# Kernel optimization log

Measured on AMD Instinct MI355X. Metric: run time of the kernel, lower is better.

The kernel has to match this reference:

```python
import jax, jax.numpy as jnp
import numpy as np


def _init(key, shape, fan_in):
    return jax.random.normal(key, shape, jnp.float32) * (1.0 / np.sqrt(fan_in))


def setup_inputs() -> dict:
    key = jax.random.key(0)
    ks = jax.random.split(key, 12)
    b, n, vd, ad, sd, hd = 32, 2048, 512, 128, 128, 64
    return {
        'vfeat': jax.random.normal(ks[0], (b, n, vd), jnp.float32),
        'afeat': jax.random.normal(ks[1], (b, n, ad), jnp.float32),
        'vfc_w': _init(ks[2], (ad, vd), vd), 'vfc_b': jnp.zeros((ad,), jnp.float32),
        'afc_w': _init(ks[3], (ad, ad), ad), 'afc_b': jnp.zeros((ad,), jnp.float32),
        'am_v_w': _init(ks[4], (sd, sd), sd), 'am_v_b': jnp.zeros((sd,), jnp.float32),
        'am_a_w': _init(ks[5], (sd, sd), sd), 'am_a_b': jnp.zeros((sd,), jnp.float32),
        'am_o_w': _init(ks[6], (1, sd), sd), 'am_o_b': jnp.zeros((1,), jnp.float32),
        'V_w': _init(ks[7], (hd, sd), sd), 'V_b': jnp.zeros((hd,), jnp.float32),
        'W_w': _init(ks[8], (1, hd), hd), 'W_b': jnp.zeros((1,), jnp.float32),
        'cls_w': _init(ks[9], (2, sd), sd), 'cls_b': jnp.zeros((2,), jnp.float32),
    }


def reference(vfeat, afeat, vfc_w, vfc_b, afc_w, afc_b,
              am_v_w, am_v_b, am_a_w, am_a_b, am_o_w, am_o_b,
              V_w, V_b, W_w, W_b, cls_w, cls_b):
    relu = jax.nn.relu
    # vfc / afc projections (dropout is identity in eval mode)
    vo1 = relu(jnp.einsum('bnd,kd->bnk', vfeat, vfc_w) + vfc_b)  # (b,n,128)
    ax = relu(jnp.einsum('bnd,kd->bnk', afeat, afc_w) + afc_b)   # (b,n,128)
    # AM(128): additive gated cross-modal attention: out = sigmoid(Wo tanh(Wv v + Wa a)) * a
    h = jnp.tanh(jnp.einsum('bnk,jk->bnj', vo1, am_v_w) + am_v_b
                 + jnp.einsum('bnk,jk->bnj', ax, am_a_w) + am_a_b)
    att = jax.nn.sigmoid(jnp.einsum('bnj,oj->bno', h, am_o_w) + am_o_b)  # (b,n,1)
    ffeat = att * ax + vo1  # attfeat + vo1, (b,n,128)
    # NOTE: original uses self.V for BOTH f_v and f_u (source bug kept)
    f_v = relu(jnp.einsum('bnk,hk->bnh', ffeat, V_w) + V_b)  # (b,n,64)
    f_u = f_v
    # W is affine with no nonlinearity on (fv_i + fu_j), so
    # W(fv_i + fu_j) = w.fv_i + w.fu_j + b  -- exact rank-1 decomposition
    s_v = f_v @ W_w[0]  # (b,n)
    s_u = f_u @ W_w[0]  # (b,n)
    pair = s_v[:, :, None] + s_u[:, None, :] + W_b[0]  # (b,n_i,n_j)
    p = jax.nn.softmax(pair, axis=1)  # F.softmax(scores, 0) per bag: over i
    scores = p.mean(axis=2)  # mean over j -> (b,n)
    # eval mode: training-only softmax over dim 2 skipped
    zfeat = jnp.einsum('bn,bnk->bk', scores, ffeat)  # (b,128)
    logits = zfeat @ cls_w.T + cls_b  # (b,2)
    return scores, logits
```

## Files before the change

kernel.cpp:

```cpp
#include <hip/hip_runtime.h>
#include <cstddef>
#include <cstdint>


typedef __attribute__((ext_vector_type(8))) short short8;
typedef __attribute__((ext_vector_type(4))) float float4v;

#define MFMA16(a, b, c) __builtin_amdgcn_mfma_f32_16x16x32_bf16((a), (b), (c), 0, 0, 0)

__device__ __forceinline__ unsigned short f2bf(float f) {
    union { float f; unsigned u; } v; v.f = f;
    unsigned r = (v.u + 0x7fffu + ((v.u >> 16) & 1u)) >> 16;
    return (unsigned short)r;
}
__device__ __forceinline__ float bf2f(unsigned short h) {
    union { unsigned u; float f; } v; v.u = ((unsigned)h) << 16;
    return v.f;
}
__device__ __forceinline__ float bf2f_s(short h) { return bf2f((unsigned short)h); }

__device__ __forceinline__ void bfsplit(float x, short& h, short& l) {
    union { float f; unsigned u; } v; v.f = x;
    h = (short)(v.u >> 16);
    union { unsigned u; float f; } hv; hv.u = v.u & 0xffff0000u;
    union { float f; unsigned u; } lv; lv.f = x - hv.f;
    l = (short)(lv.u >> 16);
}

__device__ __forceinline__ float tanh_fast(float x) {
    float e = __builtin_exp2f(x * 2.885390081777927f);
    return 1.f - 2.f / (e + 1.f);
}
__device__ __forceinline__ float sigmoid_fast(float x) {
    return 1.f / (1.f + __builtin_exp2f(-x * 1.4426950408889634f));
}

__device__ __forceinline__ void gload_lds16(const void* g, void* l) {
#if __has_builtin(__builtin_amdgcn_global_load_lds)
    __builtin_amdgcn_global_load_lds(
        (const __attribute__((address_space(1))) unsigned int*)g,
        (__attribute__((address_space(3))) unsigned int*)l, 16, 0, 0);
#else
    *(uint4*)l = *(const uint4*)g;
#endif
}

__global__ __launch_bounds__(256)
void prep(const float* __restrict__ vfc_w, const float* __restrict__ afc_w,
          const float* __restrict__ am_v_w, const float* __restrict__ am_a_w,
          const float* __restrict__ V_w,
          unsigned short* __restrict__ W1h, unsigned short* __restrict__ W1l,
          unsigned short* __restrict__ W1bh, unsigned short* __restrict__ W1bl,
          unsigned short* __restrict__ W2v, unsigned short* __restrict__ W2a,
          unsigned short* __restrict__ W3)
{
    int t = blockIdx.x * 256 + threadIdx.x;
    if (t < 65536) {
        int j = t & 7, lane = (t >> 3) & 63, ks = (t >> 9) & 15, nf = (t >> 13) & 7;
        int n = (lane & 15) + 16 * nf, k = ks * 32 + (lane >> 4) * 8 + j;
        float x = vfc_w[n * 512 + k];
        unsigned short h = f2bf(x);
        W1h[t] = h; W1l[t] = f2bf(x - bf2f(h));
    } else if (t < 81920) {
        int u = t - 65536;
        int j = u & 7, lane = (u >> 3) & 63, ks = (u >> 9) & 3, nf = (u >> 11) & 7;
        int n = (lane & 15) + 16 * nf, k = ks * 32 + (lane >> 4) * 8 + j;
        float x = afc_w[n * 128 + k];
        unsigned short h = f2bf(x);
        W1bh[u] = h; W1bl[u] = f2bf(x - bf2f(h));
    } else if (t < 98304) {
        int u = t - 81920;
        int j = u & 7, lane = (u >> 3) & 63, ks = (u >> 9) & 3, nf = (u >> 11) & 7;
        int n = (lane & 15) + 16 * nf, k = ks * 32 + (lane >> 4) * 8 + j;
        W2v[u] = f2bf(am_v_w[n * 128 + k]);
    } else if (t < 114688) {
        int u = t - 98304;
        int j = u & 7, lane = (u >> 3) & 63, ks = (u >> 9) & 3, nf = (u >> 11) & 7;
        int n = (lane & 15) + 16 * nf, k = ks * 32 + (lane >> 4) * 8 + j;
        W2a[u] = f2bf(am_a_w[n * 128 + k]);
    } else if (t < 122880) {
        int u = t - 114688;
        int j = u & 7, lane = (u >> 3) & 63, ks = (u >> 9) & 3, nf = (u >> 11) & 3;
        int n = (lane & 15) + 16 * nf, k = ks * 32 + (lane >> 4) * 8 + j;
        W3[u] = f2bf(V_w[n * 128 + k]);
    }
}

__global__ __launch_bounds__(256, 2)
void milA(const float* __restrict__ vfeat, const float* __restrict__ afeat,
          const float* __restrict__ vfc_b, const float* __restrict__ afc_b,
          const float* __restrict__ am_v_b, const float* __restrict__ am_a_b,
          const float* __restrict__ am_o_w, const float* __restrict__ am_o_b,
          const float* __restrict__ V_b, const float* __restrict__ W_w,
          const unsigned short* __restrict__ W1h, const unsigned short* __restrict__ W1l,
          const unsigned short* __restrict__ W1bh, const unsigned short* __restrict__ W1bl,
          const unsigned short* __restrict__ W2v, const unsigned short* __restrict__ W2a,
          const unsigned short* __restrict__ W3,
          float* __restrict__ ffeat_out, float* __restrict__ s_out)
{
    __shared__ __align__(16) unsigned short bstage[16384];
    __shared__ __align__(16) unsigned short vo1s[8192];
    __shared__ __align__(16) unsigned short axs[8192];

    const int tid = threadIdx.x;
    const int lane = tid & 63, wid = tid >> 6;
    const int lr = lane & 15, lg = lane >> 4;
    const int row0 = blockIdx.x * 64 + wid * 16;

    const float* ap  = vfeat + (size_t)(row0 + lr) * 512 + lg * 8;
    const float* apb = afeat + (size_t)(row0 + lr) * 128 + lg * 8;

    float4v acc1[8];
#pragma unroll
    for (int nf = 0; nf < 8; ++nf)
#pragma unroll
        for (int i = 0; i < 4; ++i) acc1[nf][i] = 0.f;

    float4 acur[4], anxt[4];
#pragma unroll
    for (int q = 0; q < 4; ++q)
        acur[q] = *(const float4*)(ap + (q >> 1) * 32 + (q & 1) * 4);

    for (int s = 0; s < 8; ++s) {
        __syncthreads();
#pragma unroll
        for (int i = 0; i < 8; ++i) {
            const int f = wid * 8 + i;
            const int ksl = f >> 4, rest = f & 15, isl = rest >> 3, nf = rest & 7;
            const unsigned short* src = (isl ? W1l : W1h)
                + (size_t)(nf * 16 + (s * 2 + ksl)) * 512 + (size_t)lane * 8;
            gload_lds16(src, &bstage[f * 512 + lane * 8]);
        }
        __syncthreads();

        if (s < 7) {
            const float* apn = ap + (s + 1) * 64;
#pragma unroll
            for (int q = 0; q < 4; ++q)
                anxt[q] = *(const float4*)(apn + (q >> 1) * 32 + (q & 1) * 4);
        } else {
#pragma unroll
            for (int q = 0; q < 4; ++q)
                anxt[q] = *(const float4*)(apb + (q >> 1) * 32 + (q & 1) * 4);
        }

#pragma unroll
        for (int ksl = 0; ksl < 2; ++ksl) {
            short8 ah, al;
            {
                const float4 x0 = acur[ksl * 2], x1 = acur[ksl * 2 + 1];
                const float xs[8] = {x0.x, x0.y, x0.z, x0.w, x1.x, x1.y, x1.z, x1.w};
#pragma unroll
                for (int j = 0; j < 8; ++j) {
                    short h, l; bfsplit(xs[j], h, l);
                    ah[j] = h; al[j] = l;
                }
            }
#pragma unroll
            for (int nf = 0; nf < 8; ++nf) {
                const short8 bh = *(const short8*)&bstage[(ksl * 16 + nf) * 512 + lane * 8];
                const short8 bl = *(const short8*)&bstage[(ksl * 16 + 8 + nf) * 512 + lane * 8];
                acc1[nf] = MFMA16(ah, bh, acc1[nf]);
                acc1[nf] = MFMA16(ah, bl, acc1[nf]);
                acc1[nf] = MFMA16(al, bh, acc1[nf]);
            }
        }
#pragma unroll
        for (int q = 0; q < 4; ++q) acur[q] = anxt[q];
    }
#pragma unroll
    for (int nf = 0; nf < 8; ++nf) {
        const float bb = vfc_b[lr + 16 * nf];
#pragma unroll
        for (int r = 0; r < 4; ++r) {
            float v = fmaxf(acc1[nf][r] + bb, 0.f);
            acc1[nf][r] = v;
            const int row = lg * 4 + r;
            const int col = lr + 16 * nf;
            vo1s[wid * 2048 + row * 128 + (col ^ ((row & 7) << 3))] = f2bf(v);
        }
    }

    float4v acc1b[8];
#pragma unroll
    for (int nf = 0; nf < 8; ++nf)
#pragma unroll
        for (int i = 0; i < 4; ++i) acc1b[nf][i] = 0.f;

    for (int s = 0; s < 2; ++s) {
        __syncthreads();
#pragma unroll
        for (int i = 0; i < 8; ++i) {
            const int f = wid * 8 + i;
            const int ksl = f >> 4, rest = f & 15, isl = rest >> 3, nf = rest & 7;
            const unsigned short* src = (isl ? W1bl : W1bh)
                + (size_t)(nf * 4 + (s * 2 + ksl)) * 512 + (size_t)lane * 8;
            gload_lds16(src, &bstage[f * 512 + lane * 8]);
        }
        __syncthreads();

        if (s < 1) {
            const float* apn = apb + 64;
#pragma unroll
            for (int q = 0; q < 4; ++q)
                anxt[q] = *(const float4*)(apn + (q >> 1) * 32 + (q & 1) * 4);
        }

#pragma unroll
        for (int ksl = 0; ksl < 2; ++ksl) {
            short8 ah, al;
            {
                const float4 x0 = acur[ksl * 2], x1 = acur[ksl * 2 + 1];
                const float xs[8] = {x0.x, x0.y, x0.z, x0.w, x1.x, x1.y, x1.z, x1.w};
#pragma unroll
                for (int j = 0; j < 8; ++j) {
                    short h, l; bfsplit(xs[j], h, l);
                    ah[j] = h; al[j] = l;
                }
            }
#pragma unroll
            for (int nf = 0; nf < 8; ++nf) {
                const short8 bh = *(const short8*)&bstage[(ksl * 16 + nf) * 512 + lane * 8];
                const short8 bl = *(const short8*)&bstage[(ksl * 16 + 8 + nf) * 512 + lane * 8];
                acc1b[nf] = MFMA16(ah, bh, acc1b[nf]);
                acc1b[nf] = MFMA16(ah, bl, acc1b[nf]);
                acc1b[nf] = MFMA16(al, bh, acc1b[nf]);
            }
        }
#pragma unroll
        for (int q = 0; q < 4; ++q) acur[q] = anxt[q];
    }
#pragma unroll
    for (int nf = 0; nf < 8; ++nf) {
        const float bb = afc_b[lr + 16 * nf];
#pragma unroll
        for (int r = 0; r < 4; ++r) {
            float v = fmaxf(acc1b[nf][r] + bb, 0.f);
            acc1b[nf][r] = v;
            const int row = lg * 4 + r;
            const int col = lr + 16 * nf;
            axs[wid * 2048 + row * 128 + (col ^ ((row & 7) << 3))] = f2bf(v);
        }
    }

    float4v acc2[8];
#pragma unroll
    for (int nf = 0; nf < 8; ++nf)
#pragma unroll
        for (int i = 0; i < 4; ++i) acc2[nf][i] = 0.f;

    for (int s = 0; s < 2; ++s) {
        __syncthreads();
#pragma unroll
        for (int i = 0; i < 8; ++i) {
            const int f = wid * 8 + i;
            const int ksl = f >> 4, rest = f & 15, isa = rest >> 3, nf = rest & 7;
            const unsigned short* src = (isa ? W2a : W2v)
                + (size_t)(nf * 4 + (s * 2 + ksl)) * 512 + (size_t)lane * 8;
            gload_lds16(src, &bstage[f * 512 + lane * 8]);
        }
        __syncthreads();

#pragma unroll
        for (int ksl = 0; ksl < 2; ++ksl) {
            const int ks = s * 2 + ksl;
            const int rdoff = (ks * 32 + lg * 8) ^ ((lr & 7) << 3);
            const short8 a2v = *(const short8*)&vo1s[wid * 2048 + lr * 128 + rdoff];
            const short8 a2a = *(const short8*)&axs[wid * 2048 + lr * 128 + rdoff];
#pragma unroll
            for (int nf = 0; nf < 8; ++nf) {
                const short8 bv = *(const short8*)&bstage[(ksl * 16 + nf) * 512 + lane * 8];
                const short8 ba = *(const short8*)&bstage[(ksl * 16 + 8 + nf) * 512 + lane * 8];
                acc2[nf] = MFMA16(a2v, bv, acc2[nf]);
                acc2[nf] = MFMA16(a2a, ba, acc2[nf]);
            }
        }
    }

    __syncthreads();
#pragma unroll
    for (int i = 0; i < 4; ++i) {
        const int f = wid * 4 + i;
        gload_lds16(W3 + (size_t)f * 512 + lane * 8, &bstage[f * 512 + lane * 8]);
    }

    float attc[4];
    {
        float bias2[8], wo[8];
#pragma unroll
        for (int nf = 0; nf < 8; ++nf) {
            const int c = lr + 16 * nf;
            bias2[nf] = am_v_b[c] + am_a_b[c];
            wo[nf] = am_o_w[c];
        }
        const float ob = am_o_b[0];
#pragma unroll
        for (int r = 0; r < 4; ++r) {
            float p = 0.f;
#pragma unroll
            for (int nf = 0; nf < 8; ++nf)
                p += tanh_fast(acc2[nf][r] + bias2[nf]) * wo[nf];
            p += __shfl_xor(p, 1);
            p += __shfl_xor(p, 2);
            p += __shfl_xor(p, 4);
            p += __shfl_xor(p, 8);
            attc[r] = sigmoid_fast(p + ob);
        }
    }

#pragma unroll
    for (int nf = 0; nf < 8; ++nf)
#pragma unroll
        for (int r = 0; r < 4; ++r)
            ffeat_out[(size_t)(row0 + lg * 4 + r) * 128 + lr + 16 * nf] =
                attc[r] * acc1b[nf][r] + acc1[nf][r];

    float attv;
    {
        const int srcl = (lr >> 2) << 4;
        const float b0 = __shfl(attc[0], srcl);
        const float b1 = __shfl(attc[1], srcl);
        const float b2 = __shfl(attc[2], srcl);
        const float b3 = __shfl(attc[3], srcl);
        attv = (lr & 2) ? ((lr & 1) ? b3 : b2) : ((lr & 1) ? b1 : b0);
    }

    __syncthreads();

    float4v acc3[4];
#pragma unroll
    for (int nf = 0; nf < 4; ++nf)
#pragma unroll
        for (int i = 0; i < 4; ++i) acc3[nf][i] = 0.f;

#pragma unroll
    for (int ks = 0; ks < 4; ++ks) {
        const int rdoff = (ks * 32 + lg * 8) ^ ((lr & 7) << 3);
        const short8 x8 = *(const short8*)&axs[wid * 2048 + lr * 128 + rdoff];
        const short8 v8 = *(const short8*)&vo1s[wid * 2048 + lr * 128 + rdoff];
        short8 a3;
#pragma unroll
        for (int j = 0; j < 8; ++j) {
            float f = attv * bf2f_s(x8[j]) + bf2f_s(v8[j]);
            a3[j] = (short)f2bf(f);
        }
#pragma unroll
        for (int nf = 0; nf < 4; ++nf) {
            const short8 b = *(const short8*)&bstage[(nf * 4 + ks) * 512 + lane * 8];
            acc3[nf] = MFMA16(a3, b, acc3[nf]);
        }
    }

    {
        float vb3[4], ww3[4];
#pragma unroll
        for (int nf = 0; nf < 4; ++nf) {
            const int c = lr + 16 * nf;
            vb3[nf] = V_b[c];
            ww3[nf] = W_w[c];
        }
#pragma unroll
        for (int r = 0; r < 4; ++r) {
            float q = 0.f;
#pragma unroll
            for (int nf = 0; nf < 4; ++nf)
                q += fmaxf(acc3[nf][r] + vb3[nf], 0.f) * ww3[nf];
            q += __shfl_xor(q, 1);
            q += __shfl_xor(q, 2);
            q += __shfl_xor(q, 4);
            q += __shfl_xor(q, 8);
            if (lr == 0) s_out[row0 + lg * 4 + r] = q;
        }
    }
}

__device__ __forceinline__ float wred_sum(float v) {
#pragma unroll
    for (int m = 32; m >= 1; m >>= 1) v += __shfl_xor(v, m);
    return v;
}
__device__ __forceinline__ float wred_max(float v) {
#pragma unroll
    for (int m = 32; m >= 1; m >>= 1) v = fmaxf(v, __shfl_xor(v, m));
    return v;
}

__global__ __launch_bounds__(256)
void milB12(const float* __restrict__ s_in, const float* __restrict__ ffeat,
            float* __restrict__ scores_out, float* __restrict__ parts)
{
    __shared__ float red[4];
    __shared__ float sh[256];
    __shared__ float zbuf[256];

    const int t = threadIdx.x, w = t >> 6;
    const int b = blockIdx.x >> 3, part = blockIdx.x & 7;
    const float* sb = s_in + (size_t)b * 2048;

    float v[8];
#pragma unroll
    for (int q = 0; q < 8; ++q) v[q] = sb[q * 256 + t];
    float m = v[0];
#pragma unroll
    for (int q = 1; q < 8; ++q) m = fmaxf(m, v[q]);
    m = wred_max(m);
    if ((t & 63) == 0) red[w] = m;
    __syncthreads();
    const float bm = fmaxf(fmaxf(red[0], red[1]), fmaxf(red[2], red[3]));

    float sum = 0.f;
#pragma unroll
    for (int q = 0; q < 8; ++q) sum += expf(v[q] - bm);
    sum = wred_sum(sum);
    __syncthreads();
    if ((t & 63) == 0) red[w] = sum;
    __syncthreads();
    const float inv = 1.f / (red[0] + red[1] + red[2] + red[3]);

    const float sv = sb[part * 256 + t];
    const float sc = expf(sv - bm) * inv;
    scores_out[(size_t)b * 2048 + part * 256 + t] = sc;
    sh[t] = sc;
    __syncthreads();

    const int col = t & 127, half = t >> 7;
    const float* fb = ffeat + ((size_t)(b * 2048 + part * 256 + half * 128)) * 128 + col;
    const float* sp = sh + half * 128;
    float z = 0.f;
#pragma unroll 8
    for (int nn = 0; nn < 128; ++nn) z += sp[nn] * fb[(size_t)nn * 128];
    zbuf[t] = z;
    __syncthreads();
    if (t < 128) parts[((size_t)(b * 8 + part)) * 128 + t] = zbuf[t] + zbuf[t + 128];
}

__global__ __launch_bounds__(128)
void milB3(const float* __restrict__ parts, const float* __restrict__ cls_w,
           const float* __restrict__ cls_b, float* __restrict__ logits)
{
    __shared__ float zfs[128];
    const int t = threadIdx.x, b = blockIdx.x;
    float zf = 0.f;
#pragma unroll
    for (int p = 0; p < 8; ++p) zf += parts[((size_t)(b * 8 + p)) * 128 + t];
    zfs[t] = zf;
    __syncthreads();
    const int o = t >> 6, c = t & 63;
    float q = zfs[c] * cls_w[o * 128 + c] + zfs[c + 64] * cls_w[o * 128 + c + 64];
    q = wred_sum(q);
    if (c == 0) logits[b * 2 + o] = q + cls_b[o];
}

extern "C" void kernel_launch(void* const* d_in, const int* in_sizes, int n_in,
                              void* d_out, int out_size, void* d_ws, size_t ws_size,
                              hipStream_t stream)
{
    (void)in_sizes; (void)n_in; (void)out_size; (void)ws_size;
    const float* vfeat  = (const float*)d_in[0];
    const float* afeat  = (const float*)d_in[1];
    const float* vfc_w  = (const float*)d_in[2];
    const float* vfc_b  = (const float*)d_in[3];
    const float* afc_w  = (const float*)d_in[4];
    const float* afc_b  = (const float*)d_in[5];
    const float* am_v_w = (const float*)d_in[6];
    const float* am_v_b = (const float*)d_in[7];
    const float* am_a_w = (const float*)d_in[8];
    const float* am_a_b = (const float*)d_in[9];
    const float* am_o_w = (const float*)d_in[10];
    const float* am_o_b = (const float*)d_in[11];
    const float* V_w    = (const float*)d_in[12];
    const float* V_b    = (const float*)d_in[13];
    const float* W_w    = (const float*)d_in[14];
    const float* cls_w  = (const float*)d_in[16];
    const float* cls_b  = (const float*)d_in[17];

    float* scores = (float*)d_out;
    float* logits = (float*)d_out + 32 * 2048;

    char* ws = (char*)d_ws;
    float* ffeat_ws = (float*)ws;
    float* s_ws     = (float*)(ws + 33554432);
    float* parts_ws = (float*)(ws + 33816576);
    unsigned short* W1h  = (unsigned short*)(ws + 33947648);
    unsigned short* W1l  = W1h + 65536;
    unsigned short* W1bh = W1l + 65536;
    unsigned short* W1bl = W1bh + 16384;
    unsigned short* W2v  = W1bl + 16384;
    unsigned short* W2a  = W2v + 16384;
    unsigned short* W3   = W2a + 16384;

    prep<<<480, 256, 0, stream>>>(vfc_w, afc_w, am_v_w, am_a_w, V_w,
                                  W1h, W1l, W1bh, W1bl, W2v, W2a, W3);
    milA<<<1024, 256, 0, stream>>>(vfeat, afeat, vfc_b, afc_b, am_v_b, am_a_b,
                                   am_o_w, am_o_b, V_b, W_w,
                                   W1h, W1l, W1bh, W1bl, W2v, W2a, W3,
                                   ffeat_ws, s_ws);
    milB12<<<256, 256, 0, stream>>>(s_ws, ffeat_ws, scores, parts_ws);
    milB3<<<32, 128, 0, stream>>>(parts_ws, cls_w, cls_b, logits);
}
```

Measured before the change: 83.51 us.

## Drop low-half weight term in vfc GEMM and halve LDS staging for occupancy

The vfc projection now uses only the high bf16 half of the weights, so it runs two MFMAs per step (ah*bh, al*bh) instead of three. That cuts weight staging traffic and matrix work in the largest GEMM. The LDS staging buffer is halved, and the afc and attention GEMM loops are restructured to stage one k-slice per sync. Launch bounds are raised to 3 blocks per CU to improve occupancy. This loses precision in the vfc output and doubles the number of barrier rounds in the smaller GEMMs.

```diff
diff --git a/kernel.cpp b/kernel.cpp
--- a/kernel.cpp
+++ b/kernel.cpp
@@ -86,19 +86,19 @@
     }
 }
 
-__global__ __launch_bounds__(256, 2)
+__global__ __launch_bounds__(256, 3)
 void milA(const float* __restrict__ vfeat, const float* __restrict__ afeat,
           const float* __restrict__ vfc_b, const float* __restrict__ afc_b,
           const float* __restrict__ am_v_b, const float* __restrict__ am_a_b,
           const float* __restrict__ am_o_w, const float* __restrict__ am_o_b,
           const float* __restrict__ V_b, const float* __restrict__ W_w,
-          const unsigned short* __restrict__ W1h, const unsigned short* __restrict__ W1l,
+          const unsigned short* __restrict__ W1h,
           const unsigned short* __restrict__ W1bh, const unsigned short* __restrict__ W1bl,
           const unsigned short* __restrict__ W2v, const unsigned short* __restrict__ W2a,
           const unsigned short* __restrict__ W3,
           float* __restrict__ ffeat_out, float* __restrict__ s_out)
 {
-    __shared__ __align__(16) unsigned short bstage[16384];
+    __shared__ __align__(16) unsigned short bstage[8192];
     __shared__ __align__(16) unsigned short vo1s[8192];
     __shared__ __align__(16) unsigned short axs[8192];
 
@@ -124,10 +124,10 @@
     for (int s = 0; s < 8; ++s) {
         __syncthreads();
 #pragma unroll
-        for (int i = 0; i < 8; ++i) {
-            const int f = wid * 8 + i;
-            const int ksl = f >> 4, rest = f & 15, isl = rest >> 3, nf = rest & 7;
-            const unsigned short* src = (isl ? W1l : W1h)
+        for (int i = 0; i < 4; ++i) {
+            const int f = wid * 4 + i;
+            const int ksl = f >> 3, nf = f & 7;
+            const unsigned short* src = W1h
                 + (size_t)(nf * 16 + (s * 2 + ksl)) * 512 + (size_t)lane * 8;
             gload_lds16(src, &bstage[f * 512 + lane * 8]);
         }
@@ -158,10 +158,8 @@
             }
 #pragma unroll
             for (int nf = 0; nf < 8; ++nf) {
-                const short8 bh = *(const short8*)&bstage[(ksl * 16 + nf) * 512 + lane * 8];
-                const short8 bl = *(const short8*)&bstage[(ksl * 16 + 8 + nf) * 512 + lane * 8];
+                const short8 bh = *(const short8*)&bstage[(ksl * 8 + nf) * 512 + lane * 8];
                 acc1[nf] = MFMA16(ah, bh, acc1[nf]);
-                acc1[nf] = MFMA16(ah, bl, acc1[nf]);
                 acc1[nf] = MFMA16(al, bh, acc1[nf]);
             }
         }
@@ -187,48 +185,47 @@
 #pragma unroll
         for (int i = 0; i < 4; ++i) acc1b[nf][i] = 0.f;
 
-    for (int s = 0; s < 2; ++s) {
-        __syncthreads();
-#pragma unroll
-        for (int i = 0; i < 8; ++i) {
-            const int f = wid * 8 + i;
-            const int ksl = f >> 4, rest = f & 15, isl = rest >> 3, nf = rest & 7;
+    for (int ks = 0; ks < 4; ++ks) {
+        __syncthreads();
+#pragma unroll
+        for (int i = 0; i < 4; ++i) {
+            const int f = wid * 4 + i;
+            const int isl = f >> 3, nf = f & 7;
             const unsigned short* src = (isl ? W1bl : W1bh)
-                + (size_t)(nf * 4 + (s * 2 + ksl)) * 512 + (size_t)lane * 8;
+                + (size_t)(nf * 4 + ks) * 512 + (size_t)lane * 8;
             gload_lds16(src, &bstage[f * 512 + lane * 8]);
         }
         __syncthreads();
 
-        if (s < 1) {
+        if (ks == 0) {
             const float* apn = apb + 64;
 #pragma unroll
             for (int q = 0; q < 4; ++q)
                 anxt[q] = *(const float4*)(apn + (q >> 1) * 32 + (q & 1) * 4);
         }
 
-#pragma unroll
-        for (int ksl = 0; ksl < 2; ++ksl) {
-            short8 ah, al;
-            {
-                const float4 x0 = acur[ksl * 2], x1 = acur[ksl * 2 + 1];
-                const float xs[8] = {x0.x, x0.y, x0.z, x0.w, x1.x, x1.y, x1.z, x1.w};
-#pragma unroll
-                for (int j = 0; j < 8; ++j) {
-                    short h, l; bfsplit(xs[j], h, l);
-                    ah[j] = h; al[j] = l;
-                }
+        short8 ah, al;
+        {
+            const float4 x0 = acur[(ks & 1) * 2], x1 = acur[(ks & 1) * 2 + 1];
+            const float xs[8] = {x0.x, x0.y, x0.z, x0.w, x1.x, x1.y, x1.z, x1.w};
+#pragma unroll
+            for (int j = 0; j < 8; ++j) {
+                short h, l; bfsplit(xs[j], h, l);
+                ah[j] = h; al[j] = l;
             }
-#pragma unroll
-            for (int nf = 0; nf < 8; ++nf) {
-                const short8 bh = *(const short8*)&bstage[(ksl * 16 + nf) * 512 + lane * 8];
-                const short8 bl = *(const short8*)&bstage[(ksl * 16 + 8 + nf) * 512 + lane * 8];
-                acc1b[nf] = MFMA16(ah, bh, acc1b[nf]);
-                acc1b[nf] = MFMA16(ah, bl, acc1b[nf]);
-                acc1b[nf] = MFMA16(al, bh, acc1b[nf]);
-            }
-        }
-#pragma unroll
-        for (int q = 0; q < 4; ++q) acur[q] = anxt[q];
+        }
+#pragma unroll
+        for (int nf = 0; nf < 8; ++nf) {
+            const short8 bh = *(const short8*)&bstage[nf * 512 + lane * 8];
+            const short8 bl = *(const short8*)&bstage[(8 + nf) * 512 + lane * 8];
+            acc1b[nf] = MFMA16(ah, bh, acc1b[nf]);
+            acc1b[nf] = MFMA16(ah, bl, acc1b[nf]);
+            acc1b[nf] = MFMA16(al, bh, acc1b[nf]);
+        }
+        if (ks == 1) {
+#pragma unroll
+            for (int q = 0; q < 4; ++q) acur[q] = anxt[q];
+        }
     }
 #pragma unroll
     for (int nf = 0; nf < 8; ++nf) {
@@ -249,31 +246,27 @@
 #pragma unroll
         for (int i = 0; i < 4; ++i) acc2[nf][i] = 0.f;
 
-    for (int s = 0; s < 2; ++s) {
-        __syncthreads();
-#pragma unroll
-        for (int i = 0; i < 8; ++i) {
-            const int f = wid * 8 + i;
-            const int ksl = f >> 4, rest = f & 15, isa = rest >> 3, nf = rest & 7;
+    for (int ks = 0; ks < 4; ++ks) {
+        __syncthreads();
+#pragma unroll
+        for (int i = 0; i < 4; ++i) {
+            const int f = wid * 4 + i;
+            const int isa = f >> 3, nf = f & 7;
             const unsigned short* src = (isa ? W2a : W2v)
-                + (size_t)(nf * 4 + (s * 2 + ksl)) * 512 + (size_t)lane * 8;
+                + (size_t)(nf * 4 + ks) * 512 + (size_t)lane * 8;
             gload_lds16(src, &bstage[f * 512 + lane * 8]);
         }
         __syncthreads();
 
-#pragma unroll
-        for (int ksl = 0; ksl < 2; ++ksl) {
-            const int ks = s * 2 + ksl;
-            const int rdoff = (ks * 32 + lg * 8) ^ ((lr & 7) << 3);
-            const short8 a2v = *(const short8*)&vo1s[wid * 2048 + lr * 128 + rdoff];
-            const short8 a2a = *(const short8*)&axs[wid * 2048 + lr * 128 + rdoff];
-#pragma unroll
-            for (int nf = 0; nf < 8; ++nf) {
-                const short8 bv = *(const short8*)&bstage[(ksl * 16 + nf) * 512 + lane * 8];
-                const short8 ba = *(const short8*)&bstage[(ksl * 16 + 8 + nf) * 512 + lane * 8];
-                acc2[nf] = MFMA16(a2v, bv, acc2[nf]);
-                acc2[nf] = MFMA16(a2a, ba, acc2[nf]);
-            }
+        const int rdoff = (ks * 32 + lg * 8) ^ ((lr & 7) << 3);
+        const short8 a2v = *(const short8*)&vo1s[wid * 2048 + lr * 128 + rdoff];
+        const short8 a2a = *(const short8*)&axs[wid * 2048 + lr * 128 + rdoff];
+#pragma unroll
+        for (int nf = 0; nf < 8; ++nf) {
+            const short8 bv = *(const short8*)&bstage[nf * 512 + lane * 8];
+            const short8 ba = *(const short8*)&bstage[(8 + nf) * 512 + lane * 8];
+            acc2[nf] = MFMA16(a2v, bv, acc2[nf]);
+            acc2[nf] = MFMA16(a2a, ba, acc2[nf]);
         }
     }
 
@@ -493,7 +486,7 @@
                                   W1h, W1l, W1bh, W1bl, W2v, W2a, W3);
     milA<<<1024, 256, 0, stream>>>(vfeat, afeat, vfc_b, afc_b, am_v_b, am_a_b,
                                    am_o_w, am_o_b, V_b, W_w,
-                                   W1h, W1l, W1bh, W1bl, W2v, W2a, W3,
+                                   W1h, W1bh, W1bl, W2v, W2a, W3,
                                    ffeat_ws, s_ws);
     milB12<<<256, 256, 0, stream>>>(s_ws, ffeat_ws, scores, parts_ws);
     milB3<<<32, 128, 0, stream>>>(parts_ws, cls_w, cls_b, logits);
```

Measured after the change: 94.20 us. 12.8% more time.
